# Optimization experiments

Measured on AMD Instinct MI355X. Metric: run time of the kernel, lower is better.

The kernel has to match this reference:

```python
import jax, jax.numpy as jnp
import numpy as np


def setup_inputs() -> dict:
    key = jax.random.key(0)
    ks = jax.random.split(key, 8)
    B, C, H, W = 16, 512, 96, 96
    Cr = C // 8
    s = 0.02
    return {
        "x": jax.random.normal(ks[0], (B, C, H, W), jnp.float32),
        "Wq": jax.random.normal(ks[1], (Cr, C), jnp.float32) * s,
        "bq": jax.random.normal(ks[2], (Cr,), jnp.float32) * s,
        "Wk": jax.random.normal(ks[3], (Cr, C), jnp.float32) * s,
        "bk": jax.random.normal(ks[4], (Cr,), jnp.float32) * s,
        "Wv": jax.random.normal(ks[5], (C, C), jnp.float32) * s,
        "bv": jax.random.normal(ks[6], (C,), jnp.float32) * s,
        "gamma": jax.random.normal(ks[7], (1,), jnp.float32) * 0.1,
    }


def _conv1x1(x, W, b):
    # 1x1 conv == channel contraction: [B,C,H,W] x [O,C] -> [B,O,H,W]
    return jnp.einsum('bchw,oc->bohw', x, W) + b[None, :, None, None]


def reference(x, Wq, bq, Wk, bk, Wv, bv, gamma):
    B, C, H, W = x.shape
    q = _conv1x1(x, Wq, bq)   # [B,Cr,H,W]
    k = _conv1x1(x, Wk, bk)   # [B,Cr,H,W]
    v = _conv1x1(x, Wv, bv)   # [B,C,H,W]

    # energy along column (vertical): query at (i,w), keys at (j,w) -> [B,H,W,H]
    eh = jnp.einsum('bciw,bcjw->biwj', q, k)
    # energy along row (horizontal): query at (h,i), keys at (h,j) -> [B,H,W,W]
    ew = jnp.einsum('bchi,bchj->bhij', q, k)

    attn = jax.nn.softmax(jnp.concatenate([eh, ew], axis=-1), axis=-1)  # [B,H,W,H+W]
    ah = attn[..., :H]   # [B,H,W,H]
    aw = attn[..., H:]   # [B,H,W,W]

    out_h = jnp.einsum('bcjw,biwj->bciw', v, ah)  # vertical aggregation
    out_w = jnp.einsum('bchj,bhij->bchi', v, aw)  # horizontal aggregation
    out = out_h + out_w
    return gamma[0] * out + x
```

## Files before the change

### kernel.cpp

```cpp
#include <hip/hip_runtime.h>
#include <hip/hip_bf16.h>

#define DI __device__ __forceinline__

typedef short bf16x8 __attribute__((ext_vector_type(8)));
typedef float f32x4 __attribute__((ext_vector_type(4)));
typedef unsigned short u16;
typedef u16 u16x2 __attribute__((ext_vector_type(2)));
typedef u16 u16x4 __attribute__((ext_vector_type(4)));
typedef u16 u16x8 __attribute__((ext_vector_type(8)));

#define B_ 16
#define C_ 512
#define CR_ 64
#define H_ 96
#define HW_ 9216
#define K_ 512

DI float b2f(u16 u){ unsigned v = ((unsigned)u)<<16; float f; __builtin_memcpy(&f,&v,4); return f; }
DI u16 f2b(float f){ unsigned v; __builtin_memcpy(&v,&f,4); v += 0x7fff + ((v>>16)&1); return (u16)(v>>16); }

DI void gload16(const void* g, void* l){
  __builtin_amdgcn_global_load_lds((const __attribute__((address_space(1))) unsigned*)g,
                                   (__attribute__((address_space(3))) unsigned*)l, 16, 0, 0);
}

__global__ __launch_bounds__(256) void k_pack(const float* __restrict__ Wq, const float* __restrict__ bq,
    const float* __restrict__ Wk, const float* __restrict__ bk,
    const float* __restrict__ Wv, const float* __restrict__ bv,
    u16* __restrict__ Wcat, float* __restrict__ bcat){
  int gid = blockIdx.x*256 + threadIdx.x;
  int o = gid >> 9, c = gid & 511;
  float w = (o < 64) ? Wq[o*512 + c] : (o < 128) ? Wk[(o-64)*512 + c] : Wv[(o-128)*512 + c];
  Wcat[gid] = f2b(w);
  if (c == 0) bcat[o] = (o < 64) ? bq[o] : (o < 128) ? bk[o-64] : bv[o-128];
}

__global__ __launch_bounds__(256) void k_xt(const float* __restrict__ x, u16* __restrict__ xt){
  int bx = blockIdx.x;
  int pt = bx % 144; int ct = (bx/144) & 7; int b = bx / (144*8);
  __shared__ u16 T[64*80];
  const float* xb = x + (size_t)b*C_*HW_ + (size_t)(ct*64)*HW_ + pt*64;
  for (int it = threadIdx.x; it < 1024; it += 256){
    int px4 = it & 15, r = it >> 4;
    f32x4 f4 = *(const f32x4*)(xb + (size_t)r*HW_ + px4*4);
    #pragma unroll
    for (int e=0;e<4;++e) T[(px4*4 + e)*80 + r] = f2b(f4[e]);
  }
  __syncthreads();
  u16* xtb = xt + (size_t)b*HW_*K_ + (size_t)(pt*64)*K_ + ct*64;
  for (int it = threadIdx.x; it < 512; it += 256){
    int c8 = it & 7, p = it >> 3;
    u16x8 o;
    #pragma unroll
    for (int e=0;e<8;++e) o[e] = T[p*80 + c8*8 + e];
    *(u16x8*)(xtb + (size_t)p*K_ + c8*8) = o;
  }
}

__global__ __launch_bounds__(512) void k_qkv(const u16* __restrict__ Wcat, const float* __restrict__ bcat,
    const u16* __restrict__ xt, u16* __restrict__ q, u16* __restrict__ k, u16* __restrict__ v){
  int bx = blockIdx.x;
  int wg = (bx & 7)*360 + (bx >> 3);
  int mt = wg % 5; int rest = wg / 5; int nt = rest % 36; int b = rest / 36;
  __shared__ u16 As[128*64];
  __shared__ u16 Bs[256*64];
  int lane = threadIdx.x & 63, wid = threadIdx.x >> 6;
  int wr = wid >> 2, wc = wid & 3;
  const u16* xb = xt + (size_t)b*HW_*K_ + (size_t)nt*256*K_;
  const u16* Ab = Wcat + (size_t)mt*128*K_;

  f32x4 acc[4][4];
  #pragma unroll
  for (int i=0;i<4;++i)
    #pragma unroll
    for (int j=0;j<4;++j) acc[i][j] = (f32x4){0.f,0.f,0.f,0.f};

  for (int kt=0; kt<8; ++kt){
    int k0 = kt*64;
    __syncthreads();
    #pragma unroll
    for (int i=0;i<2;++i){
      int dest = ((wid*2 + i)<<10);
      int byteL = dest + (lane<<4);
      int row = byteL >> 7;
      int slog = ((byteL >> 4) & 7) ^ (row & 7);
      gload16(Ab + (size_t)row*K_ + (k0 + slog*8), (char*)As + dest);
    }
    #pragma unroll
    for (int i=0;i<4;++i){
      int dest = ((wid*4 + i)<<10);
      int byteL = dest + (lane<<4);
      int row = byteL >> 7;
      int slog = ((byteL >> 4) & 7) ^ (row & 7);
      gload16(xb + (size_t)row*K_ + (k0 + slog*8), (char*)Bs + dest);
    }
    __syncthreads();
    bf16x8 af[4][2], bfr[4][2];
    #pragma unroll
    for (int f=0; f<4; ++f){
      #pragma unroll
      for (int kk=0; kk<2; ++kk){
        int sl = kk*4 + (lane >> 4);
        int ra = wr*64 + f*16 + (lane & 15);
        af[f][kk]  = *(const bf16x8*)((const char*)As + ra*128 + ((sl ^ (ra & 7))<<4));
        int rb = wc*64 + f*16 + (lane & 15);
        bfr[f][kk] = *(const bf16x8*)((const char*)Bs + rb*128 + ((sl ^ (rb & 7))<<4));
      }
    }
    #pragma unroll
    for (int fm=0; fm<4; ++fm)
      #pragma unroll
      for (int fn=0; fn<4; ++fn)
        #pragma unroll
        for (int kk=0; kk<2; ++kk)
          acc[fm][fn] = __builtin_amdgcn_mfma_f32_16x16x32_bf16(af[fm][kk], bfr[fn][kk], acc[fm][fn], 0, 0, 0);
  }

  u16* Cs = Bs;
  int r4 = lane >> 4, cl = lane & 15;
  #pragma unroll
  for (int h=0; h<2; ++h){
    __syncthreads();
    if ((wc >> 1) == h){
      #pragma unroll
      for (int fm=0; fm<4; ++fm)
        #pragma unroll
        for (int j=0; j<4; ++j){
          int row = wr*64 + fm*16 + r4*4 + j;
          float bias = bcat[mt*128 + row];
          int sx = ((row>>2)&3)<<1;
          #pragma unroll
          for (int fn=0; fn<4; ++fn){
            int col = (wc&1)*64 + fn*16 + cl;
            Cs[row*128 + (((col>>3) ^ sx)<<3) + (col&7)] = f2b(acc[fm][fn][j] + bias);
          }
        }
    }
    __syncthreads();
    #pragma unroll
    for (int i=0; i<4; ++i){
      int chunk = i*512 + threadIdx.x;
      int row = chunk >> 4, c8 = chunk & 15;
      int sx = ((row>>2)&3)<<1;
      u16x8 val = *(const u16x8*)&Cs[row*128 + (c8<<3)];
      int colb = c8 ^ sx;
      int o = mt*128 + row;
      int n = nt*256 + h*128 + colb*8;
      u16* dst;
      if (o < 64)       dst = q + ((size_t)b*CR_ + o)*HW_ + n;
      else if (o < 128) dst = k + ((size_t)b*CR_ + (o-64))*HW_ + n;
      else              dst = v + ((size_t)b*C_ + (o-128))*HW_ + n;
      *(u16x8*)dst = val;
    }
  }
}

__global__ __launch_bounds__(256) void k_tr(const u16* __restrict__ q, const u16* __restrict__ kk,
    const u16* __restrict__ v, u16* __restrict__ qt, u16* __restrict__ kt, u16* __restrict__ vt){
  int bx = blockIdx.x;
  int ch = bx % 640; int b = bx / 640;
  const u16* src; u16* dst;
  if (ch < 64)      { src = q  + ((size_t)b*CR_ + ch)*HW_;     dst = qt + ((size_t)b*CR_ + ch)*HW_; }
  else if (ch < 128){ src = kk + ((size_t)b*CR_ + ch-64)*HW_;  dst = kt + ((size_t)b*CR_ + ch-64)*HW_; }
  else              { src = v  + ((size_t)b*C_ + ch-128)*HW_;  dst = vt + ((size_t)b*C_ + ch-128)*HW_; }
  __shared__ u16 T[96*128];
  for (int it = threadIdx.x; it < 1152; it += 256){
    int h = it / 12, c8 = it % 12;
    u16x8 v8 = *(const u16x8*)(src + h*96 + c8*8);
    int sp = (h >> 3) ^ (c8 & 7);
    #pragma unroll
    for (int e = 0; e < 8; ++e){
      int w = c8*8 + e;
      T[w*128 + sp*8 + (h & 7)] = v8[e];
    }
  }
  __syncthreads();
  for (int it = threadIdx.x; it < 1152; it += 256){
    int w = it / 12, h8 = it % 12;
    int sp = h8 ^ ((w >> 3) & 7);
    u16x8 o = *(const u16x8*)&T[w*128 + sp*8];
    *(u16x8*)(dst + (size_t)w*96 + h8*8) = o;
  }
}

__global__ __launch_bounds__(256) void k_scores(const u16* __restrict__ q, const u16* __restrict__ k,
    const u16* __restrict__ qt, const u16* __restrict__ kt, u16* __restrict__ att){
  int bx = blockIdx.x;
  int p = bx % 96; int b = (bx/96) & 15; int mode = bx / 1536;
  __shared__ float Qs[64*96];
  __shared__ float Ks[64*96];
  const u16* qsrc; const u16* ksrc;
  if (mode == 0){ qsrc = qt + (size_t)b*CR_*HW_ + p*96; ksrc = kt + (size_t)b*CR_*HW_ + p*96; }
  else          { qsrc = q  + (size_t)b*CR_*HW_ + p*96; ksrc = k  + (size_t)b*CR_*HW_ + p*96; }
  for (int u = threadIdx.x; u < 64*12; u += 256){
    int c = u / 12, ch = u % 12;
    u16x8 a = *(const u16x8*)(qsrc + (size_t)c*HW_ + ch*8);
    u16x8 d = *(const u16x8*)(ksrc + (size_t)c*HW_ + ch*8);
    #pragma unroll
    for (int e=0;e<8;++e){ Qs[c*96 + ch*8 + e] = b2f(a[e]); Ks[c*96 + ch*8 + e] = b2f(d[e]); }
  }
  __syncthreads();
  int ti = threadIdx.x >> 4, tj = threadIdx.x & 15;
  float acc[6][6];
  #pragma unroll
  for (int a2=0;a2<6;++a2)
    #pragma unroll
    for (int b2=0;b2<6;++b2) acc[a2][b2] = 0.f;
  for (int c=0;c<64;++c){
    float qv[6], kv[6];
    #pragma unroll
    for (int a2=0;a2<6;++a2){ qv[a2] = Qs[c*96 + ti + 16*a2]; kv[a2] = Ks[c*96 + tj + 16*a2]; }
    #pragma unroll
    for (int a2=0;a2<6;++a2)
      #pragma unroll
      for (int b2=0;b2<6;++b2) acc[a2][b2] += qv[a2]*kv[b2];
  }
  for (int a2=0;a2<6;++a2){
    int i = ti + 16*a2;
    for (int b2=0;b2<6;++b2){
      int j = tj + 16*b2;
      size_t idx = (mode==0) ? ((size_t)((b*96 + i)*96 + p))*192 + j
                             : ((size_t)((b*96 + p)*96 + i))*192 + 96 + j;
      att[idx] = f2b(acc[a2][b2]);
    }
  }
}

__global__ __launch_bounds__(256) void k_softmax(u16* __restrict__ att){
  int row = blockIdx.x*8 + (threadIdx.x >> 5);
  int sub = threadIdx.x & 31;
  u16* r = att + (size_t)row*192 + sub*6;
  u16x2 a = *(u16x2*)r, b = *(u16x2*)(r+2), c = *(u16x2*)(r+4);
  float v0=b2f(a[0]),v1=b2f(a[1]),v2=b2f(b[0]),v3=b2f(b[1]),v4=b2f(c[0]),v5=b2f(c[1]);
  float m = fmaxf(fmaxf(fmaxf(v0,v1),fmaxf(v2,v3)),fmaxf(v4,v5));
  #pragma unroll
  for (int off=16; off; off>>=1) m = fmaxf(m, __shfl_xor(m, off));
  float e0=__expf(v0-m),e1=__expf(v1-m),e2=__expf(v2-m),e3=__expf(v3-m),e4=__expf(v4-m),e5=__expf(v5-m);
  float s = ((e0+e1)+(e2+e3))+(e4+e5);
  #pragma unroll
  for (int off=16; off; off>>=1) s += __shfl_xor(s, off);
  float inv = 1.0f/s;
  a[0]=f2b(e0*inv); a[1]=f2b(e1*inv); b[0]=f2b(e2*inv); b[1]=f2b(e3*inv); c[0]=f2b(e4*inv); c[1]=f2b(e5*inv);
  *(u16x2*)r = a; *(u16x2*)(r+2) = b; *(u16x2*)(r+4) = c;
}

__global__ __launch_bounds__(512) void k_outh(u16* vo, const u16* __restrict__ att){
  int bx = blockIdx.x; int w = bx % 96, b = bx / 96;
  __shared__ u16 Ah[96*104];
  for (int u = threadIdx.x; u < 96*48; u += 512){
    int i = u/48, jc = u%48;
    *(u16x2*)&Ah[i*104 + jc*2] = *(const u16x2*)(att + ((size_t)((b*96 + i)*96 + w))*192 + jc*2);
  }
  __syncthreads();
  int lane = threadIdx.x & 63, wid = threadIdx.x >> 6;
  int cl = lane & 15, r4 = lane >> 4;
  f32x4 acc[4][6];
  #pragma unroll
  for (int i=0;i<4;++i)
    #pragma unroll
    for (int j=0;j<6;++j) acc[i][j] = (f32x4){0.f,0.f,0.f,0.f};
  u16* vb = vo + (size_t)b*C_*HW_ + (size_t)w*96;
  #pragma unroll
  for (int kt=0; kt<3; ++kt){
    int kof = kt*32 + r4*8;
    bf16x8 a[4], bb[6];
    #pragma unroll
    for (int fm=0; fm<4; ++fm){
      int c = wid*64 + fm*16 + cl;
      a[fm] = *(const bf16x8*)(vb + (size_t)c*HW_ + kof);
    }
    #pragma unroll
    for (int fn=0; fn<6; ++fn)
      bb[fn] = *(const bf16x8*)&Ah[(fn*16 + cl)*104 + kof];
    #pragma unroll
    for (int fm=0; fm<4; ++fm)
      #pragma unroll
      for (int fn=0; fn<6; ++fn)
        acc[fm][fn] = __builtin_amdgcn_mfma_f32_16x16x32_bf16(a[fm], bb[fn], acc[fm][fn], 0, 0, 0);
  }
  for (int fm=0; fm<4; ++fm)
    for (int fn=0; fn<6; ++fn)
      for (int j=0;j<4;++j){
        int c = wid*64 + fm*16 + r4*4 + j;
        int i = fn*16 + cl;
        vb[(size_t)c*HW_ + i] = f2b(acc[fm][fn][j]);
      }
}

__global__ __launch_bounds__(512) void k_outw(u16* vo, const u16* __restrict__ att){
  int bx = blockIdx.x; int h = bx % 96, b = bx / 96;
  __shared__ u16 Aw[96*104];
  for (int u = threadIdx.x; u < 96*48; u += 512){
    int i = u/48, jc = u%48;
    *(u16x2*)&Aw[i*104 + jc*2] = *(const u16x2*)(att + ((size_t)((b*96 + h)*96 + i))*192 + 96 + jc*2);
  }
  __syncthreads();
  int lane = threadIdx.x & 63, wid = threadIdx.x >> 6;
  int cl = lane & 15, r4 = lane >> 4;
  f32x4 acc[4][6];
  #pragma unroll
  for (int i=0;i<4;++i)
    #pragma unroll
    for (int j=0;j<6;++j) acc[i][j] = (f32x4){0.f,0.f,0.f,0.f};
  u16* vb = vo + (size_t)b*C_*HW_ + (size_t)h*96;
  #pragma unroll
  for (int kt=0; kt<3; ++kt){
    int kof = kt*32 + r4*8;
    bf16x8 a[4], bb[6];
    #pragma unroll
    for (int fm=0; fm<4; ++fm){
      int c = wid*64 + fm*16 + cl;
      a[fm] = *(const bf16x8*)(vb + (size_t)c*HW_ + kof);
    }
    #pragma unroll
    for (int fn=0; fn<6; ++fn)
      bb[fn] = *(const bf16x8*)&Aw[(fn*16 + cl)*104 + kof];
    #pragma unroll
    for (int fm=0; fm<4; ++fm)
      #pragma unroll
      for (int fn=0; fn<6; ++fn)
        acc[fm][fn] = __builtin_amdgcn_mfma_f32_16x16x32_bf16(a[fm], bb[fn], acc[fm][fn], 0, 0, 0);
  }
  for (int fm=0; fm<4; ++fm)
    for (int fn=0; fn<6; ++fn)
      for (int j=0;j<4;++j){
        int c = wid*64 + fm*16 + r4*4 + j;
        int i = fn*16 + cl;
        vb[(size_t)c*HW_ + i] = f2b(acc[fm][fn][j]);
      }
}

__global__ __launch_bounds__(256) void k_final(const u16* oh, const u16* ow,
    const float* __restrict__ x, const float* __restrict__ gp, float* __restrict__ out){
  int bx = blockIdx.x; int c = bx & 511; int b = bx >> 9;
  size_t base = ((size_t)b*C_ + c)*HW_;
  const u16* ohc = oh + base;
  const u16* owc = ow + base;
  __shared__ u16 T[96*100];
  for (int it = threadIdx.x; it < 288; it += 256){
    int w4 = it % 24, i8 = it / 24;
    const u16* src = ohc + (w4*4)*96 + i8*8;
    u16x8 r0 = *(const u16x8*)(src);
    u16x8 r1 = *(const u16x8*)(src + 96);
    u16x8 r2 = *(const u16x8*)(src + 192);
    u16x8 r3 = *(const u16x8*)(src + 288);
    #pragma unroll
    for (int e = 0; e < 8; ++e){
      u16x4 t = {r0[e], r1[e], r2[e], r3[e]};
      *(u16x4*)&T[(i8*8 + e)*100 + w4*4] = t;
    }
  }
  __syncthreads();
  float g = gp[0];
  for (int it = threadIdx.x; it < 2304; it += 256){
    int i = it / 24, w4 = it % 24; int w = w4*4;
    u16x4 t4 = *(const u16x4*)&T[i*100 + w4*4];
    u16x4 o4 = *(const u16x4*)(owc + i*96 + w);
    f32x4 x4 = *(const f32x4*)(x + base + i*96 + w);
    f32x4 r;
    #pragma unroll
    for (int e=0;e<4;++e) r[e] = g*(b2f(t4[e]) + b2f(o4[e])) + x4[e];
    *(f32x4*)(out + base + i*96 + w) = r;
  }
}

extern "C" void kernel_launch(void* const* d_in, const int* in_sizes, int n_in,
                              void* d_out, int out_size, void* d_ws, size_t ws_size,
                              hipStream_t stream) {
  (void)in_sizes; (void)n_in; (void)out_size; (void)ws_size;
  const float* x  = (const float*)d_in[0];
  const float* Wq = (const float*)d_in[1];
  const float* bq = (const float*)d_in[2];
  const float* Wk = (const float*)d_in[3];
  const float* bk = (const float*)d_in[4];
  const float* Wv = (const float*)d_in[5];
  const float* bv = (const float*)d_in[6];
  const float* gm = (const float*)d_in[7];
  float* out = (float*)d_out;
  char* ws = (char*)d_ws;

  u16*  Wcat = (u16*)(ws);
  float* bcat= (float*)(ws + 655360);
  u16*  q    = (u16*)(ws + 659456);
  u16*  k    = (u16*)(ws + 19533824);
  u16*  qt   = (u16*)(ws + 38408192);
  u16*  kt   = (u16*)(ws + 57282560);
  u16*  v    = (u16*)(ws + 76156928);
  u16*  att  = (u16*)(ws + 227151872);
  u16*  vt   = (u16*)(ws + 283774976);
  u16*  xt   = (u16*)d_out;

  k_pack   <<<1280, 256, 0, stream>>>(Wq,bq,Wk,bk,Wv,bv,Wcat,bcat);
  k_xt     <<<18432,256, 0, stream>>>(x, xt);
  k_qkv    <<<2880, 512, 0, stream>>>(Wcat,bcat,xt,q,k,v);
  k_tr     <<<10240,256, 0, stream>>>(q,k,v,qt,kt,vt);
  k_scores <<<3072, 256, 0, stream>>>(q,k,qt,kt,att);
  k_softmax<<<18432,256, 0, stream>>>(att);
  k_outh   <<<1536, 512, 0, stream>>>(vt,att);
  k_outw   <<<1536, 512, 0, stream>>>(v,att);
  k_final  <<<8192, 256, 0, stream>>>(vt,v,x,gm,out);
}
```

Before: 740.2 us.

## Fuse x transpose and bf16 conversion into QKV projection GEMM

Removes the standalone kernel that transposed x into a bf16 pixel-major buffer. The QKV GEMM now loads fp32 x directly, packs pairs to bf16 with a hardware convert instruction, and writes swizzled tiles into LDS. This saves the intermediate write and re-read and one launch. In exchange, each output-channel tile re-reads fp32 x, and the B operand loads become synchronous register loads instead of direct-to-LDS loads.

```diff
diff --git a/kernel.cpp b/kernel.cpp
--- a/kernel.cpp
+++ b/kernel.cpp
@@ -6,6 +6,7 @@
 typedef short bf16x8 __attribute__((ext_vector_type(8)));
 typedef float f32x4 __attribute__((ext_vector_type(4)));
 typedef unsigned short u16;
+typedef unsigned u32x2 __attribute__((ext_vector_type(2)));
 typedef u16 u16x2 __attribute__((ext_vector_type(2)));
 typedef u16 u16x4 __attribute__((ext_vector_type(4)));
 typedef u16 u16x8 __attribute__((ext_vector_type(8)));
@@ -19,6 +20,12 @@
 
 DI float b2f(u16 u){ unsigned v = ((unsigned)u)<<16; float f; __builtin_memcpy(&f,&v,4); return f; }
 DI u16 f2b(float f){ unsigned v; __builtin_memcpy(&v,&f,4); v += 0x7fff + ((v>>16)&1); return (u16)(v>>16); }
+
+DI unsigned cvtpk(float lo, float hi){
+  unsigned r;
+  asm("v_cvt_pk_bf16_f32 %0, %1, %2" : "=v"(r) : "v"(lo), "v"(hi));
+  return r;
+}
 
 DI void gload16(const void* g, void* l){
   __builtin_amdgcn_global_load_lds((const __attribute__((address_space(1))) unsigned*)g,
@@ -36,30 +43,8 @@
   if (c == 0) bcat[o] = (o < 64) ? bq[o] : (o < 128) ? bk[o-64] : bv[o-128];
 }
 
-__global__ __launch_bounds__(256) void k_xt(const float* __restrict__ x, u16* __restrict__ xt){
-  int bx = blockIdx.x;
-  int pt = bx % 144; int ct = (bx/144) & 7; int b = bx / (144*8);
-  __shared__ u16 T[64*80];
-  const float* xb = x + (size_t)b*C_*HW_ + (size_t)(ct*64)*HW_ + pt*64;
-  for (int it = threadIdx.x; it < 1024; it += 256){
-    int px4 = it & 15, r = it >> 4;
-    f32x4 f4 = *(const f32x4*)(xb + (size_t)r*HW_ + px4*4);
-    #pragma unroll
-    for (int e=0;e<4;++e) T[(px4*4 + e)*80 + r] = f2b(f4[e]);
-  }
-  __syncthreads();
-  u16* xtb = xt + (size_t)b*HW_*K_ + (size_t)(pt*64)*K_ + ct*64;
-  for (int it = threadIdx.x; it < 512; it += 256){
-    int c8 = it & 7, p = it >> 3;
-    u16x8 o;
-    #pragma unroll
-    for (int e=0;e<8;++e) o[e] = T[p*80 + c8*8 + e];
-    *(u16x8*)(xtb + (size_t)p*K_ + c8*8) = o;
-  }
-}
-
 __global__ __launch_bounds__(512) void k_qkv(const u16* __restrict__ Wcat, const float* __restrict__ bcat,
-    const u16* __restrict__ xt, u16* __restrict__ q, u16* __restrict__ k, u16* __restrict__ v){
+    const float* __restrict__ x, u16* __restrict__ q, u16* __restrict__ k, u16* __restrict__ v){
   int bx = blockIdx.x;
   int wg = (bx & 7)*360 + (bx >> 3);
   int mt = wg % 5; int rest = wg / 5; int nt = rest % 36; int b = rest / 36;
@@ -67,8 +52,12 @@
   __shared__ u16 Bs[256*64];
   int lane = threadIdx.x & 63, wid = threadIdx.x >> 6;
   int wr = wid >> 2, wc = wid & 3;
-  const u16* xb = xt + (size_t)b*HW_*K_ + (size_t)nt*256*K_;
+  int P0 = nt*256;
+  const float* xc = x + (size_t)b*C_*HW_ + P0;
   const u16* Ab = Wcat + (size_t)mt*128*K_;
+
+  int C4 = threadIdx.x & 15;
+  int P4 = threadIdx.x >> 4;
 
   f32x4 acc[4][4];
   #pragma unroll
@@ -87,13 +76,21 @@
       int slog = ((byteL >> 4) & 7) ^ (row & 7);
       gload16(Ab + (size_t)row*K_ + (k0 + slog*8), (char*)As + dest);
     }
-    #pragma unroll
-    for (int i=0;i<4;++i){
-      int dest = ((wid*4 + i)<<10);
-      int byteL = dest + (lane<<4);
-      int row = byteL >> 7;
-      int slog = ((byteL >> 4) & 7) ^ (row & 7);
-      gload16(xb + (size_t)row*K_ + (k0 + slog*8), (char*)Bs + dest);
+    f32x4 ra[4], rb[4];
+    #pragma unroll
+    for (int I=0;I<4;++I){
+      const float* rp = xc + (size_t)(k0 + C4*4 + I)*HW_;
+      ra[I] = *(const f32x4*)(rp + P4*4);
+      rb[I] = *(const f32x4*)(rp + P4*4 + 128);
+    }
+    #pragma unroll
+    for (int j=0;j<4;++j){
+      int pl = P4*4 + j;
+      int byteo = pl*128 + ((((C4>>1) ^ (pl&7))<<4)) + ((C4&1)<<3);
+      *(u32x2*)((char*)Bs + byteo) = (u32x2){cvtpk(ra[0][j], ra[1][j]), cvtpk(ra[2][j], ra[3][j])};
+      int pl2 = pl + 128;
+      int byteo2 = pl2*128 + ((((C4>>1) ^ (pl2&7))<<4)) + ((C4&1)<<3);
+      *(u32x2*)((char*)Bs + byteo2) = (u32x2){cvtpk(rb[0][j], rb[1][j]), cvtpk(rb[2][j], rb[3][j])};
     }
     __syncthreads();
     bf16x8 af[4][2], bfr[4][2];
@@ -102,10 +99,10 @@
       #pragma unroll
       for (int kk=0; kk<2; ++kk){
         int sl = kk*4 + (lane >> 4);
-        int ra = wr*64 + f*16 + (lane & 15);
-        af[f][kk]  = *(const bf16x8*)((const char*)As + ra*128 + ((sl ^ (ra & 7))<<4));
-        int rb = wc*64 + f*16 + (lane & 15);
-        bfr[f][kk] = *(const bf16x8*)((const char*)Bs + rb*128 + ((sl ^ (rb & 7))<<4));
+        int ra_ = wr*64 + f*16 + (lane & 15);
+        af[f][kk]  = *(const bf16x8*)((const char*)As + ra_*128 + ((sl ^ (ra_ & 7))<<4));
+        int rb_ = wc*64 + f*16 + (lane & 15);
+        bfr[f][kk] = *(const bf16x8*)((const char*)Bs + rb_*128 + ((sl ^ (rb_ & 7))<<4));
       }
     }
     #pragma unroll
@@ -389,11 +386,9 @@
   u16*  v    = (u16*)(ws + 76156928);
   u16*  att  = (u16*)(ws + 227151872);
   u16*  vt   = (u16*)(ws + 283774976);
-  u16*  xt   = (u16*)d_out;
 
   k_pack   <<<1280, 256, 0, stream>>>(Wq,bq,Wk,bk,Wv,bv,Wcat,bcat);
-  k_xt     <<<18432,256, 0, stream>>>(x, xt);
-  k_qkv    <<<2880, 512, 0, stream>>>(Wcat,bcat,xt,q,k,v);
+  k_qkv    <<<2880, 512, 0, stream>>>(Wcat,bcat,x,q,k,v);
   k_tr     <<<10240,256, 0, stream>>>(q,k,v,qt,kt,vt);
   k_scores <<<3072, 256, 0, stream>>>(q,k,qt,kt,att);
   k_softmax<<<18432,256, 0, stream>>>(att);
```

Result: slower. 776.1 us (+4.9%).
